# Kernel tuning notes

Hardware: AMD Instinct MI355X
Metric: run time of the kernel (lower is better)

The kernel has to match this reference:

```python
import jax, jax.numpy as jnp
import numpy as np
from jax import lax

B, C, T = 512, 63, 250          # batch, EEG channels, timepoints
S = 10                           # number of subjects
E = 4                            # emb_size of CNN projection
HID, PROJ = 184, 1024            # hidden_dim (=4*46), embed_dim
EPS = 1e-5
DN = ('NCHW', 'OIHW', 'NCHW')


def setup_inputs() -> dict:
    key = jax.random.key(0)
    ks = jax.random.split(key, 16)
    p = {}
    p['x'] = jax.random.normal(ks[0], (B, C, T), dtype=jnp.float32)
    p['subjects'] = jax.random.randint(ks[1], (B,), 0, S, dtype=jnp.int32)
    # per-subject Linear(T, T): weight [S, T, T], bias [S, T]
    p['W_subj'] = jax.random.normal(ks[2], (S, T, T), dtype=jnp.float32) * 0.02
    p['b_subj'] = jnp.zeros((S, T), dtype=jnp.float32)
    # tsconv
    p['conv1_w'] = jax.random.normal(ks[3], (40, 1, 1, 5), dtype=jnp.float32) * 0.1
    p['conv1_b'] = jnp.zeros((40,), dtype=jnp.float32)
    p['bn1_g'] = jnp.ones((40,), dtype=jnp.float32)
    p['bn1_b'] = jnp.zeros((40,), dtype=jnp.float32)
    p['conv2_w'] = jax.random.normal(ks[4], (40, 40, C, 1), dtype=jnp.float32) * 0.02
    p['conv2_b'] = jnp.zeros((40,), dtype=jnp.float32)
    p['bn2_g'] = jnp.ones((40,), dtype=jnp.float32)
    p['bn2_b'] = jnp.zeros((40,), dtype=jnp.float32)
    # 1x1 projection conv to emb_size
    p['proj_w'] = jax.random.normal(ks[5], (E, 40, 1, 1), dtype=jnp.float32) * 0.1
    p['proj_b'] = jnp.zeros((E,), dtype=jnp.float32)
    # MLP projector
    p['fc1_w'] = jax.random.normal(ks[6], (PROJ, HID), dtype=jnp.float32) * 0.05
    p['fc1_b'] = jnp.zeros((PROJ,), dtype=jnp.float32)
    p['fc2_w'] = jax.random.normal(ks[7], (PROJ, PROJ), dtype=jnp.float32) * 0.02
    p['fc2_b'] = jnp.zeros((PROJ,), dtype=jnp.float32)
    p['ln_g'] = jnp.ones((PROJ,), dtype=jnp.float32)
    p['ln_b'] = jnp.zeros((PROJ,), dtype=jnp.float32)
    return p


def _bn(h, g, b):
    # BatchNorm2d with batch statistics over (N, H, W), NCHW layout
    mu = jnp.mean(h, axis=(0, 2, 3), keepdims=True)
    var = jnp.var(h, axis=(0, 2, 3), keepdims=True)
    return (h - mu) * lax.rsqrt(var + EPS) * g[None, :, None, None] + b[None, :, None, None]


def _avgpool_w(h, k, s):
    # average pool over last (W) dim, kernel k stride s
    summed = lax.reduce_window(h, 0.0, lax.add, (1, 1, 1, k), (1, 1, 1, s), 'VALID')
    return summed / k


def reference(x, subjects, W_subj, b_subj, conv1_w, conv1_b, bn1_g, bn1_b,
              conv2_w, conv2_b, bn2_g, bn2_b, proj_w, proj_b,
              fc1_w, fc1_b, fc2_w, fc2_b, ln_g, ln_b):
    # --- subject-conditioned linear dispatch (grouped GEMM via gather) ---
    Wg = W_subj[subjects]                      # [B, T, T]
    bg = b_subj[subjects]                      # [B, T]
    x_eeg = jnp.einsum('bct,bst->bcs', x, Wg) + bg[:, None, :]   # [B, C, T]

    # --- Spatio_Temporal_CNN ---
    h = x_eeg[:, None, :, :]                   # [B, 1, C, T]
    h = lax.conv_general_dilated(h, conv1_w, (1, 1), 'VALID', dimension_numbers=DN)
    h = h + conv1_b[None, :, None, None]       # [B, 40, C, 246]
    h = _avgpool_w(h, 17, 5)                   # [B, 40, C, 46]
    h = jax.nn.elu(_bn(h, bn1_g, bn1_b))
    h = lax.conv_general_dilated(h, conv2_w, (1, 1), 'VALID', dimension_numbers=DN)
    h = h + conv2_b[None, :, None, None]       # [B, 40, 1, 46]
    h = jax.nn.elu(_bn(h, bn2_g, bn2_b))       # dropout = identity (eval)
    h = lax.conv_general_dilated(h, proj_w, (1, 1), 'VALID', dimension_numbers=DN)
    h = h + proj_b[None, :, None, None]        # [B, E, 1, 46]
    # Rearrange 'b e h w -> b (h w) e' then flatten -> [B, 46*E] = [B, 184]
    z = jnp.transpose(h, (0, 2, 3, 1)).reshape(h.shape[0], -1)

    # --- MLP projector ---
    h1 = z @ fc1_w.T + fc1_b                   # [B, 1024]
    r = jax.nn.gelu(h1, approximate=False) @ fc2_w.T + fc2_b
    h2 = h1 + r                                # ResidualAdd (dropout = identity)
    mu = jnp.mean(h2, axis=-1, keepdims=True)
    var = jnp.var(h2, axis=-1, keepdims=True)
    return (h2 - mu) * lax.rsqrt(var + EPS) * ln_g + ln_b
```

## Files before the change

kernel.cpp:

```cpp
#include <hip/hip_runtime.h>
#include <hip/hip_bf16.h>

#define K2 2520
#define PROJ 1024
#define HID 184
#define N1F (512.f*63.f*46.f)
#define N2F (512.f*46.f)

typedef float f32x4 __attribute__((ext_vector_type(4)));
typedef short bf16x8 __attribute__((ext_vector_type(8)));
typedef unsigned short u16;
typedef unsigned short ushort8 __attribute__((ext_vector_type(8)));

__device__ __forceinline__ u16 f2bf(float f) {
    unsigned u = __builtin_bit_cast(unsigned, f);
    return (u16)((u + 0x7FFFu + ((u >> 16) & 1u)) >> 16);
}
__device__ __forceinline__ float bf2f(u16 h) {
    unsigned u = ((unsigned)h) << 16;
    return __builtin_bit_cast(float, u);
}

__global__ void kX(const float* __restrict__ W, const float* __restrict__ w2,
                   const float* __restrict__ fw1, const float* __restrict__ fw2,
                   u16* __restrict__ Wbf, u16* __restrict__ Wbf2,
                   u16* __restrict__ fwbf1, u16* __restrict__ fwbf2, float* stats) {
    int bid = blockIdx.x, tid = threadIdx.x;
    if (bid == 0 && tid < 320) stats[tid] = 0.f;
    if (bid < 2560) {
        int i = bid*256 + tid;
        int sj = i >> 16, s_ = (i >> 8) & 255, t_ = i & 255;
        float v = (s_ < 250 && t_ < 250) ? W[(size_t)sj*62500 + s_*250 + t_] : 0.f;
        Wbf[i] = f2bf(v);
    } else if (bid < 3034) {
        int i = (bid-2560)*256 + tid;
        int n = i / 2528, k = i - n*2528;
        float v = 0.f;
        if (n < 40 && k < K2) { int c = k/40, o = k - c*40; v = w2[n*K2 + o*63 + c]; }
        Wbf2[i] = f2bf(v);
    } else if (bid < 3802) {
        int i = (bid-3034)*256 + tid;
        int n = i/192, k = i - n*192;
        fwbf1[i] = f2bf(k < HID ? fw1[n*HID + k] : 0.f);
    } else {
        int i = (bid-3802)*256 + tid;
        fwbf2[i] = f2bf(fw2[i]);
    }
}

#define XS(c,s) xs[(c)*258 + (s)]
__global__ __launch_bounds__(256) void kAB(const float* __restrict__ x,
                                           const int* __restrict__ subj,
                                           const u16* __restrict__ Wbf,
                                           const float* __restrict__ bsub,
                                           const float* __restrict__ w1,
                                           const float* __restrict__ b1,
                                           u16* __restrict__ pooled,
                                           float* __restrict__ stats) {
    __shared__ float xs[32 * 258];
    __shared__ float effs[40 * 22];
    __shared__ float biasL[256];
    __shared__ float sS[4][8][5], sQ[4][8][5];
    int b = blockIdx.x, ch = blockIdx.y;
    int sj = subj[b];
    int tid = threadIdx.x;
    int wv = tid >> 6, lane = tid & 63, row = lane & 15, kg = lane >> 4;

    biasL[tid] = (tid < 250) ? bsub[sj*250 + tid] : 0.f;
    for (int i = tid; i < 840; i += 256) {
        int o = i / 21, j = i - o * 21;
        float e = 0.f;
        #pragma unroll
        for (int k = 0; k < 5; ++k) { int u = j - k; if (u >= 0 && u <= 16) e += w1[o*5+k]; }
        effs[o*22 + j] = e * (1.f / 17.f);
    }

    int cgrp = wv & 1, nfh = wv >> 1;
    int cglob = ch*32 + cgrp*16 + row;
    const float* xr = x + ((size_t)b*63 + (cglob < 63 ? cglob : 62))*250;
    const u16* Wb = Wbf + (size_t)sj*65536;
    f32x4 acc[8];
    #pragma unroll
    for (int i = 0; i < 8; ++i) acc[i] = (f32x4){0.f,0.f,0.f,0.f};
    #pragma unroll
    for (int ks = 0; ks < 8; ++ks) {
        int tb = ks*32 + kg*8;
        float av[8];
        if (ks < 7) {
            #pragma unroll
            for (int j = 0; j < 8; j += 2) { float2 v = *(const float2*)&xr[tb+j]; av[j]=v.x; av[j+1]=v.y; }
        } else {
            #pragma unroll
            for (int j = 0; j < 8; ++j) av[j] = 0.f;
            if (kg < 3) {
                #pragma unroll
                for (int j = 0; j < 8; j += 2) { float2 v = *(const float2*)&xr[tb+j]; av[j]=v.x; av[j+1]=v.y; }
            } else {
                float2 v = *(const float2*)&xr[248]; av[0]=v.x; av[1]=v.y;
            }
        }
        bf16x8 af;
        #pragma unroll
        for (int j = 0; j < 8; ++j) af[j] = (short)f2bf(av[j]);
        #pragma unroll
        for (int nf2 = 0; nf2 < 8; ++nf2) {
            int nf = nfh*8 + nf2;
            bf16x8 bv = *(const bf16x8*)(Wb + (size_t)(nf*16 + row)*256 + tb);
            acc[nf2] = __builtin_amdgcn_mfma_f32_16x16x32_bf16(af, bv, acc[nf2], 0, 0, 0);
        }
    }
    __syncthreads();
    int cw = cgrp*16 + kg*4;
    #pragma unroll
    for (int nf2 = 0; nf2 < 8; ++nf2) {
        int s = (nfh*8 + nf2)*16 + row;
        float bias = biasL[s];
        #pragma unroll
        for (int r = 0; r < 4; ++r) XS(cw + r, s) = acc[nf2][r] + bias;
    }
    __syncthreads();

    int c2 = tid >> 3, og = tid & 7;
    bool rowvalid = (ch == 0) || (c2 < 31);
    float eff[5][21];
    float bo[5];
    #pragma unroll
    for (int i = 0; i < 5; ++i) {
        int o = og*5 + i;
        bo[i] = b1[o];
        #pragma unroll
        for (int j = 0; j < 21; ++j) eff[i][j] = effs[o*22 + j];
    }
    float ssum[5] = {0.f,0.f,0.f,0.f,0.f}, ssq[5] = {0.f,0.f,0.f,0.f,0.f};
    if (rowvalid) {
        float win[21];
        #pragma unroll
        for (int j = 0; j < 21; ++j) win[j] = XS(c2, j);
        u16* prow = pooled + (size_t)b*46*K2 + (ch*32 + c2)*40 + og*5;
        for (int w = 0; w < 46; ++w) {
            float a[5];
            #pragma unroll
            for (int i = 0; i < 5; ++i) {
                float s = bo[i];
                #pragma unroll
                for (int j = 0; j < 21; ++j) s = fmaf(win[j], eff[i][j], s);
                a[i] = s;
            }
            #pragma unroll
            for (int i = 0; i < 5; ++i) {
                prow[(size_t)w*K2 + i] = f2bf(a[i]);
                ssum[i] += a[i];
                ssq[i] = fmaf(a[i], a[i], ssq[i]);
            }
            if (w < 45) {
                #pragma unroll
                for (int j2 = 0; j2 < 16; ++j2) win[j2] = win[j2+5];
                #pragma unroll
                for (int j2 = 16; j2 < 21; ++j2) win[j2] = XS(c2, 5*w + 5 + j2);
            }
        }
    }
    #pragma unroll
    for (int i = 0; i < 5; ++i) {
        float s = ssum[i], q = ssq[i];
        s += __shfl_xor(s, 8);  q += __shfl_xor(q, 8);
        s += __shfl_xor(s, 16); q += __shfl_xor(q, 16);
        s += __shfl_xor(s, 32); q += __shfl_xor(q, 32);
        if ((lane >> 3) == 0) { sS[wv][lane][i] = s; sQ[wv][lane][i] = q; }
    }
    __syncthreads();
    if (tid < 40) {
        int og2 = tid / 5, i2 = tid - og2*5;
        float s = sS[0][og2][i2] + sS[1][og2][i2] + sS[2][og2][i2] + sS[3][og2][i2];
        float q = sQ[0][og2][i2] + sQ[1][og2][i2] + sQ[2][og2][i2] + sQ[3][og2][i2];
        atomicAdd(&stats[tid], s);
        atomicAdd(&stats[40 + tid], q);
    }
}

__global__ __launch_bounds__(256) void kD(const u16* __restrict__ pooled,
                                          const u16* __restrict__ Wbf2,
                                          const float* __restrict__ b2,
                                          const float* __restrict__ g1,
                                          const float* __restrict__ bb1,
                                          const float* __restrict__ stats,
                                          float* __restrict__ out2,
                                          float* __restrict__ statw) {
    __shared__ float2 scsh[40];
    __shared__ float mrg[2][64][12];
    __shared__ float redS[2][48], redQ[2][48];
    int tid = threadIdx.x;
    if (tid < 40) {
        float mean = stats[tid] / N1F;
        float var  = stats[40 + tid] / N1F - mean * mean;
        float sc   = g1[tid] * rsqrtf(var + 1e-5f);
        scsh[tid] = make_float2(sc, bb1[tid] - mean * sc);
    }
    __syncthreads();
    int wv = tid >> 6, lane = tid & 63, row = lane & 15, kg = lane >> 4;
    int rowgrp = wv >> 1, khalf = wv & 1;
    int mbase = blockIdx.x*32 + rowgrp*16;
    const u16* pr = pooled + (size_t)(mbase + row) * K2;
    f32x4 acc[3];
    #pragma unroll
    for (int i = 0; i < 3; ++i) acc[i] = (f32x4){0.f,0.f,0.f,0.f};

    int ksBeg = khalf ? 39 : 0, ksEnd = khalf ? 79 : 39;
    for (int ks = ksBeg; ks < ksEnd; ++ks) {
        int kbase = ks*32 + kg*8;
        ushort8 cur = *(const ushort8*)&pr[kbase];
        bf16x8 bv0 = *(const bf16x8*)(Wbf2 + (size_t)(row     )*2528 + kbase);
        bf16x8 bv1 = *(const bf16x8*)(Wbf2 + (size_t)(16 + row)*2528 + kbase);
        bf16x8 bv2 = *(const bf16x8*)(Wbf2 + (size_t)(32 + row)*2528 + kbase);
        bf16x8 af;
        bool valid = (ks < 78) | (kg < 3);
        if (valid) {
            #pragma unroll
            for (int j = 0; j < 8; ++j) {
                int k = kbase + j;
                int u = (k * 1639) >> 16;
                int o = k - u*40;
                float2 sshf = scsh[o];
                float a = fmaf(bf2f(cur[j]), sshf.x, sshf.y);
                float e = a > 0.f ? a : __expf(a) - 1.f;
                af[j] = (short)f2bf(e);
            }
        } else {
            #pragma unroll
            for (int j = 0; j < 8; ++j) af[j] = 0;
        }
        acc[0] = __builtin_amdgcn_mfma_f32_16x16x32_bf16(af, bv0, acc[0], 0, 0, 0);
        acc[1] = __builtin_amdgcn_mfma_f32_16x16x32_bf16(af, bv1, acc[1], 0, 0, 0);
        acc[2] = __builtin_amdgcn_mfma_f32_16x16x32_bf16(af, bv2, acc[2], 0, 0, 0);
    }

    if (khalf) {
        #pragma unroll
        for (int nf = 0; nf < 3; ++nf)
            #pragma unroll
            for (int r = 0; r < 4; ++r) mrg[rowgrp][lane][nf*4 + r] = acc[nf][r];
    }
    __syncthreads();
    if (!khalf) {
        float sN[3] = {0.f,0.f,0.f}, qN[3] = {0.f,0.f,0.f};
        #pragma unroll
        for (int nf = 0; nf < 3; ++nf) {
            int n = nf*16 + row;
            #pragma unroll
            for (int r = 0; r < 4; ++r) acc[nf][r] += mrg[rowgrp][lane][nf*4 + r];
            if (n < 40) {
                float bias = b2[n];
                #pragma unroll
                for (int r = 0; r < 4; ++r) {
                    float v = acc[nf][r] + bias;
                    out2[(size_t)(mbase + kg*4 + r)*40 + n] = v;
                    sN[nf] += v; qN[nf] += v*v;
                }
            }
        }
        #pragma unroll
        for (int nf = 0; nf < 3; ++nf) {
            float s = sN[nf], q = qN[nf];
            s += __shfl_xor(s, 16); q += __shfl_xor(q, 16);
            s += __shfl_xor(s, 32); q += __shfl_xor(q, 32);
            if (kg == 0) { redS[rowgrp][nf*16 + row] = s; redQ[rowgrp][nf*16 + row] = q; }
        }
    }
    __syncthreads();
    if (tid < 40) {
        atomicAdd(&statw[160 + tid], redS[0][tid] + redS[1][tid]);
        atomicAdd(&statw[200 + tid], redQ[0][tid] + redQ[1][tid]);
    }
}

__global__ void kF(const float* __restrict__ out2, const float* __restrict__ stats,
                   const float* __restrict__ g2, const float* __restrict__ bb2,
                   const float* __restrict__ pw, const float* __restrict__ pb,
                   u16* __restrict__ zbf) {
    int b = blockIdx.x, t = threadIdx.x;
    __shared__ float sc[40], sh[40], pws[160];
    __shared__ float o2[1840];
    if (t < 40) {
        float mean = stats[160 + t] / N2F;
        float var  = stats[200 + t] / N2F - mean * mean;
        float s    = g2[t] * rsqrtf(var + 1e-5f);
        sc[t] = s;
        sh[t] = bb2[t] - mean * s;
    }
    if (t < 160) pws[t] = pw[t];
    for (int i = t; i < 1840; i += 256) o2[i] = out2[(size_t)b*1840 + i];
    __syncthreads();
    if (t < 192) {
        float accv = 0.f;
        if (t < HID) {
            int w = t >> 2, e = t & 3;
            accv = pb[e];
            for (int o = 0; o < 40; ++o) {
                float a = o2[w*40 + o];
                float act = a * sc[o] + sh[o];
                act = act > 0.f ? act : __expf(act) - 1.f;
                accv = fmaf(act, pws[e*40 + o], accv);
            }
        }
        zbf[(size_t)b*192 + t] = f2bf(accv);
    }
}

__global__ __launch_bounds__(256) void kG1(const u16* __restrict__ zbf, const u16* __restrict__ fwbf1,
                                           const float* __restrict__ fb,
                                           float* __restrict__ h1, u16* __restrict__ gbf) {
    int n0 = blockIdx.x * 64, m0 = blockIdx.y * 16;
    int tid = threadIdx.x, wv = tid >> 6, lane = tid & 63, row = lane & 15, kg = lane >> 4;
    const u16* zr = zbf + (size_t)(m0 + row) * 192;
    const u16* wr = fwbf1 + (size_t)(n0 + wv*16 + row) * 192;
    f32x4 acc = (f32x4){0.f,0.f,0.f,0.f};
    #pragma unroll
    for (int ks = 0; ks < 6; ++ks) {
        bf16x8 av = *(const bf16x8*)(zr + ks*32 + kg*8);
        bf16x8 bv = *(const bf16x8*)(wr + ks*32 + kg*8);
        acc = __builtin_amdgcn_mfma_f32_16x16x32_bf16(av, bv, acc, 0, 0, 0);
    }
    int n = n0 + wv*16 + row;
    float bias = fb[n];
    #pragma unroll
    for (int r = 0; r < 4; ++r) {
        int m = m0 + kg*4 + r;
        float v = acc[r] + bias;
        h1[(size_t)m*PROJ + n] = v;
        float ge = 0.5f * v * (1.f + erff(v * 0.70710678118f));
        gbf[(size_t)m*PROJ + n] = f2bf(ge);
    }
}

__global__ __launch_bounds__(256) void kG2(const u16* __restrict__ gbf, const u16* __restrict__ fwbf,
                                           const float* __restrict__ fb, const float* __restrict__ h1,
                                           float* __restrict__ h2) {
    int n0 = blockIdx.x * 32, m0 = blockIdx.y * 64;
    int tid = threadIdx.x;
    int wv = tid >> 6, lane = tid & 63, row = lane & 15, kg = lane >> 4;
    const u16* gr = gbf + (size_t)(m0 + wv*16 + row) * PROJ;
    f32x4 acc[2];
    #pragma unroll
    for (int i = 0; i < 2; ++i) acc[i] = (f32x4){0.f,0.f,0.f,0.f};
    for (int ks = 0; ks < 32; ++ks) {
        int kbase = ks*32 + kg*8;
        bf16x8 av  = *(const bf16x8*)(gr + kbase);
        bf16x8 bv0 = *(const bf16x8*)(fwbf + (size_t)(n0      + row)*PROJ + kbase);
        bf16x8 bv1 = *(const bf16x8*)(fwbf + (size_t)(n0 + 16 + row)*PROJ + kbase);
        acc[0] = __builtin_amdgcn_mfma_f32_16x16x32_bf16(av, bv0, acc[0], 0, 0, 0);
        acc[1] = __builtin_amdgcn_mfma_f32_16x16x32_bf16(av, bv1, acc[1], 0, 0, 0);
    }
    int m = m0 + wv*16 + kg*4;
    #pragma unroll
    for (int nf = 0; nf < 2; ++nf) {
        int n = n0 + nf*16 + row;
        float bias = fb[n];
        #pragma unroll
        for (int r = 0; r < 4; ++r)
            h2[(size_t)(m + r)*PROJ + n] = acc[nf][r] + bias + h1[(size_t)(m + r)*PROJ + n];
    }
}

__global__ __launch_bounds__(256) void kG3(const float* __restrict__ h2, const float* __restrict__ lg,
                                           const float* __restrict__ lb, float* __restrict__ out) {
    int b = blockIdx.x, tid = threadIdx.x;
    float4 v = *(const float4*)&h2[(size_t)b*PROJ + tid*4];
    float s = v.x + v.y + v.z + v.w;
    float q = v.x*v.x + v.y*v.y + v.z*v.z + v.w*v.w;
    __shared__ float ps[4], pq[4], mb[2];
    int wave = tid >> 6, lane = tid & 63;
    #pragma unroll
    for (int d = 32; d >= 1; d >>= 1) { s += __shfl_down(s, d); q += __shfl_down(q, d); }
    if (lane == 0) { ps[wave] = s; pq[wave] = q; }
    __syncthreads();
    if (tid == 0) {
        float S = ps[0]+ps[1]+ps[2]+ps[3], Q = pq[0]+pq[1]+pq[2]+pq[3];
        float mean = S / 1024.f, var = Q / 1024.f - mean*mean;
        mb[0] = mean; mb[1] = rsqrtf(var + 1e-5f);
    }
    __syncthreads();
    float mean = mb[0], inv = mb[1];
    float4 g4 = *(const float4*)&lg[tid*4];
    float4 b4 = *(const float4*)&lb[tid*4];
    float4 o4;
    o4.x = (v.x - mean)*inv*g4.x + b4.x;
    o4.y = (v.y - mean)*inv*g4.y + b4.y;
    o4.z = (v.z - mean)*inv*g4.z + b4.z;
    o4.w = (v.w - mean)*inv*g4.w + b4.w;
    *(float4*)&out[(size_t)b*PROJ + tid*4] = o4;
}

extern "C" void kernel_launch(void* const* d_in, const int* in_sizes, int n_in,
                              void* d_out, int out_size, void* d_ws, size_t ws_size,
                              hipStream_t stream) {
    const float* x       = (const float*)d_in[0];
    const int*   subjects= (const int*)  d_in[1];
    const float* W_subj  = (const float*)d_in[2];
    const float* b_subj  = (const float*)d_in[3];
    const float* conv1_w = (const float*)d_in[4];
    const float* conv1_b = (const float*)d_in[5];
    const float* bn1_g   = (const float*)d_in[6];
    const float* bn1_b   = (const float*)d_in[7];
    const float* conv2_w = (const float*)d_in[8];
    const float* conv2_b = (const float*)d_in[9];
    const float* bn2_g   = (const float*)d_in[10];
    const float* bn2_b   = (const float*)d_in[11];
    const float* proj_w  = (const float*)d_in[12];
    const float* proj_b  = (const float*)d_in[13];
    const float* fc1_w   = (const float*)d_in[14];
    const float* fc1_b   = (const float*)d_in[15];
    const float* fc2_w   = (const float*)d_in[16];
    const float* fc2_b   = (const float*)d_in[17];
    const float* ln_g    = (const float*)d_in[18];
    const float* ln_b    = (const float*)d_in[19];
    float* out = (float*)d_out;

    char* ws = (char*)d_ws;
    u16*   pooled = (u16*)  ws;
    float* out2   = (float*)(ws + 118702144);
    u16*   zbf    = (u16*)  (ws + 122470464);
    float* h1     = (float*)(ws + 122667072);
    float* h2     = (float*)(ws + 124764224);
    u16*   gbf    = (u16*)  (ws + 126861376);
    float* stats  = (float*)(ws + 127909952);
    u16*   Wbf    = (u16*)  (ws + 127914048);
    u16*   Wbf2   = (u16*)  (ws + 129224768);
    u16*   fwbf2  = (u16*)  (ws + 129467456);
    u16*   fwbf1  = (u16*)  (ws + 131564608);

    kX  <<<7898, 256, 0, stream>>>(W_subj, conv2_w, fc1_w, fc2_w, Wbf, Wbf2, fwbf1, fwbf2, stats);
    kAB <<<dim3(512, 2), 256, 0, stream>>>(x, subjects, Wbf, b_subj, conv1_w, conv1_b, pooled, stats);
    kD  <<<736, 256, 0, stream>>>(pooled, Wbf2, conv2_b, bn1_g, bn1_b, stats, out2, stats);
    kF  <<<512, 256, 0, stream>>>(out2, stats, bn2_g, bn2_b, proj_w, proj_b, zbf);
    kG1 <<<dim3(16, 32), 256, 0, stream>>>(zbf, fwbf1, fc1_b, h1, gbf);
    kG2 <<<dim3(32, 8), 256, 0, stream>>>(gbf, fwbf2, fc2_b, h1, h2);
    kG3 <<<512, 256, 0, stream>>>(h2, ln_g, ln_b, out);
    (void)in_sizes; (void)n_in; (void)out_size; (void)ws_size;
}
```

Baseline: 309.4 us.

## Compute fused conv1+avgpool stage with split-bf16 MFMA instead of scalar FMAs

Replaces the per-thread scalar sliding-window FMA loop for the conv1+avgpool stage with MFMA 16x16x32 bf16 matrix multiplies. Each window's 21-tap effective filter becomes a padded 48x32 B matrix, and each input row is gathered with stride 5 as an A matrix. Inputs and weights are split into high and low bf16 parts and combined in three MFMAs to keep near-fp32 accuracy. This targets the heavy VALU FMA cost in kAB, at the price of extra packing work, padded tiles and a changed output write pattern.

Result: faster. 282.5 us (-8.7%).

```diff
diff --git a/kernel.cpp b/kernel.cpp
--- a/kernel.cpp
+++ b/kernel.cpp
@@ -11,6 +11,8 @@
 typedef short bf16x8 __attribute__((ext_vector_type(8)));
 typedef unsigned short u16;
 typedef unsigned short ushort8 __attribute__((ext_vector_type(8)));
+typedef unsigned int u32;
+typedef unsigned int u32x4 __attribute__((ext_vector_type(4)));
 
 __device__ __forceinline__ u16 f2bf(float f) {
     unsigned u = __builtin_bit_cast(unsigned, f);
@@ -19,6 +21,11 @@
 __device__ __forceinline__ float bf2f(u16 h) {
     unsigned u = ((unsigned)h) << 16;
     return __builtin_bit_cast(float, u);
+}
+__device__ __forceinline__ u32 cvtpk(float lo, float hi) {
+    u32 r;
+    asm("v_cvt_pk_bf16_f32 %0, %1, %2" : "=v"(r) : "v"(lo), "v"(hi));
+    return r;
 }
 
 __global__ void kX(const float* __restrict__ W, const float* __restrict__ w2,
@@ -57,22 +64,33 @@
                                            const float* __restrict__ b1,
                                            u16* __restrict__ pooled,
                                            float* __restrict__ stats) {
-    __shared__ float xs[32 * 258];
-    __shared__ float effs[40 * 22];
+    __shared__ float xs[32*258 + 16];
+    __shared__ u16 effh[48*32] __attribute__((aligned(16)));
+    __shared__ u16 effl[48*32] __attribute__((aligned(16)));
     __shared__ float biasL[256];
-    __shared__ float sS[4][8][5], sQ[4][8][5];
+    __shared__ float sS[4][48], sQ[4][48];
     int b = blockIdx.x, ch = blockIdx.y;
     int sj = subj[b];
     int tid = threadIdx.x;
     int wv = tid >> 6, lane = tid & 63, row = lane & 15, kg = lane >> 4;
 
     biasL[tid] = (tid < 250) ? bsub[sj*250 + tid] : 0.f;
-    for (int i = tid; i < 840; i += 256) {
-        int o = i / 21, j = i - o * 21;
+    for (int i = tid; i < 1536; i += 256) {
+        int o = i >> 5, tap = i & 31;
         float e = 0.f;
-        #pragma unroll
-        for (int k = 0; k < 5; ++k) { int u = j - k; if (u >= 0 && u <= 16) e += w1[o*5+k]; }
-        effs[o*22 + j] = e * (1.f / 17.f);
+        if (o < 40 && tap < 21) {
+            #pragma unroll
+            for (int k = 0; k < 5; ++k) { int u = tap - k; if (u >= 0 && u <= 16) e += w1[o*5+k]; }
+            e *= (1.f/17.f);
+        }
+        u16 h = f2bf(e);
+        effh[i] = h;
+        effl[i] = f2bf(e - bf2f(h));
+    }
+    {
+        int r = tid >> 3, cc = tid & 7;
+        XS(r, 250 + cc) = 0.f;
+        if (tid < 16) xs[32*258 + tid] = 0.f;
     }
 
     int cgrp = wv & 1, nfh = wv >> 1;
@@ -120,59 +138,78 @@
     }
     __syncthreads();
 
-    int c2 = tid >> 3, og = tid & 7;
-    bool rowvalid = (ch == 0) || (c2 < 31);
-    float eff[5][21];
-    float bo[5];
-    #pragma unroll
-    for (int i = 0; i < 5; ++i) {
-        int o = og*5 + i;
-        bo[i] = b1[o];
-        #pragma unroll
-        for (int j = 0; j < 21; ++j) eff[i][j] = effs[o*22 + j];
-    }
-    float ssum[5] = {0.f,0.f,0.f,0.f,0.f}, ssq[5] = {0.f,0.f,0.f,0.f,0.f};
-    if (rowvalid) {
-        float win[21];
-        #pragma unroll
-        for (int j = 0; j < 21; ++j) win[j] = XS(c2, j);
-        u16* prow = pooled + (size_t)b*46*K2 + (ch*32 + c2)*40 + og*5;
-        for (int w = 0; w < 46; ++w) {
-            float a[5];
-            #pragma unroll
-            for (int i = 0; i < 5; ++i) {
-                float s = bo[i];
+    bf16x8 bvh[3], bvl[3];
+    float b1v[3];
+    bool ovalid[3];
+    #pragma unroll
+    for (int nt = 0; nt < 3; ++nt) {
+        bvh[nt] = *(const bf16x8*)(effh + (nt*16 + row)*32 + kg*8);
+        bvl[nt] = *(const bf16x8*)(effl + (nt*16 + row)*32 + kg*8);
+        int o = nt*16 + row;
+        ovalid[nt] = o < 40;
+        b1v[nt] = ovalid[nt] ? b1[o] : 0.f;
+    }
+    float ss[3] = {0.f,0.f,0.f}, sq[3] = {0.f,0.f,0.f};
+    int climit = ch ? 31 : 32;
+    for (int c2 = wv; c2 < climit; c2 += 4) {
+        f32x4 acc2[3][3];
+        #pragma unroll
+        for (int mt = 0; mt < 3; ++mt) {
+            int base = c2*258 + 5*(mt*16 + row) + kg*8;
+            float av[8];
+            #pragma unroll
+            for (int j = 0; j < 8; ++j) av[j] = xs[base + j];
+            u32x4 ph, pl;
+            #pragma unroll
+            for (int p = 0; p < 4; ++p) {
+                u32 h = cvtpk(av[2*p], av[2*p+1]);
+                float h0 = __builtin_bit_cast(float, h << 16);
+                float h1 = __builtin_bit_cast(float, h & 0xFFFF0000u);
+                ph[p] = h;
+                pl[p] = cvtpk(av[2*p] - h0, av[2*p+1] - h1);
+            }
+            bf16x8 afh = __builtin_bit_cast(bf16x8, ph);
+            bf16x8 afl = __builtin_bit_cast(bf16x8, pl);
+            #pragma unroll
+            for (int nt = 0; nt < 3; ++nt) {
+                f32x4 a = (f32x4){b1v[nt], b1v[nt], b1v[nt], b1v[nt]};
+                a = __builtin_amdgcn_mfma_f32_16x16x32_bf16(afl, bvh[nt], a, 0, 0, 0);
+                a = __builtin_amdgcn_mfma_f32_16x16x32_bf16(afh, bvl[nt], a, 0, 0, 0);
+                a = __builtin_amdgcn_mfma_f32_16x16x32_bf16(afh, bvh[nt], a, 0, 0, 0);
+                acc2[mt][nt] = a;
+            }
+        }
+        u16* prow = pooled + (size_t)b*46*K2 + (ch*32 + c2)*40;
+        #pragma unroll
+        for (int mt = 0; mt < 3; ++mt) {
+            #pragma unroll
+            for (int nt = 0; nt < 3; ++nt) {
+                if (!ovalid[nt]) continue;
+                int o = nt*16 + row;
                 #pragma unroll
-                for (int j = 0; j < 21; ++j) s = fmaf(win[j], eff[i][j], s);
-                a[i] = s;
-            }
-            #pragma unroll
-            for (int i = 0; i < 5; ++i) {
-                prow[(size_t)w*K2 + i] = f2bf(a[i]);
-                ssum[i] += a[i];
-                ssq[i] = fmaf(a[i], a[i], ssq[i]);
-            }
-            if (w < 45) {
-                #pragma unroll
-                for (int j2 = 0; j2 < 16; ++j2) win[j2] = win[j2+5];
-                #pragma unroll
-                for (int j2 = 16; j2 < 21; ++j2) win[j2] = XS(c2, 5*w + 5 + j2);
-            }
-        }
-    }
-    #pragma unroll
-    for (int i = 0; i < 5; ++i) {
-        float s = ssum[i], q = ssq[i];
-        s += __shfl_xor(s, 8);  q += __shfl_xor(q, 8);
+                for (int r = 0; r < 4; ++r) {
+                    int w = mt*16 + kg*4 + r;
+                    if (mt < 2 || w < 46) {
+                        float v = acc2[mt][nt][r];
+                        prow[(size_t)w*K2 + o] = f2bf(v);
+                        ss[nt] += v;
+                        sq[nt] = fmaf(v, v, sq[nt]);
+                    }
+                }
+            }
+        }
+    }
+    #pragma unroll
+    for (int nt = 0; nt < 3; ++nt) {
+        float s = ss[nt], q = sq[nt];
         s += __shfl_xor(s, 16); q += __shfl_xor(q, 16);
         s += __shfl_xor(s, 32); q += __shfl_xor(q, 32);
-        if ((lane >> 3) == 0) { sS[wv][lane][i] = s; sQ[wv][lane][i] = q; }
+        if (kg == 0) { sS[wv][nt*16 + row] = s; sQ[wv][nt*16 + row] = q; }
     }
     __syncthreads();
     if (tid < 40) {
-        int og2 = tid / 5, i2 = tid - og2*5;
-        float s = sS[0][og2][i2] + sS[1][og2][i2] + sS[2][og2][i2] + sS[3][og2][i2];
-        float q = sQ[0][og2][i2] + sQ[1][og2][i2] + sQ[2][og2][i2] + sQ[3][og2][i2];
+        float s = sS[0][tid]+sS[1][tid]+sS[2][tid]+sS[3][tid];
+        float q = sQ[0][tid]+sQ[1][tid]+sQ[2][tid]+sQ[3][tid];
         atomicAdd(&stats[tid], s);
         atomicAdd(&stats[40 + tid], q);
     }
```
